# Optimization experiments

Hardware: AMD Instinct MI355X
Metric: run time of the kernel (lower is better)

The kernel has to match this reference:

```python
import jax, jax.numpy as jnp
import numpy as np

D_MODEL = 1024
NUM_HEADS = 16
D_K = D_MODEL // NUM_HEADS
THETA = 10000.0
SEQ = 2048
BATCH = 2


def _rope(t, positions):
    # t: [b, h, s, d_k]; positions: [s]
    half = D_K // 2
    freqs = 1.0 / (THETA ** (jnp.arange(0, D_K, 2, dtype=jnp.float32) / D_K))  # [half]
    angles = positions.astype(jnp.float32)[:, None] * freqs[None, :]  # [s, half]
    cos = jnp.cos(angles)  # [s, half]
    sin = jnp.sin(angles)
    tr = t.reshape(t.shape[:-1] + (half, 2))  # pairs are (even, odd) interleaved
    x1, x2 = tr[..., 0], tr[..., 1]
    r1 = x1 * cos - x2 * sin
    r2 = x1 * sin + x2 * cos
    return jnp.stack([r1, r2], axis=-1).reshape(t.shape)


def setup_inputs() -> dict:
    key = jax.random.key(0)
    ks = jax.random.split(key, 5)
    std = float(np.sqrt(2.0 / (D_MODEL + D_MODEL)))
    return {
        "x": jax.random.normal(ks[0], (BATCH, SEQ, D_MODEL), dtype=jnp.float32),
        "token_positions": jnp.arange(SEQ, dtype=jnp.int64 if jax.config.jax_enable_x64 else jnp.int32),
        "wq": std * jax.random.normal(ks[1], (D_MODEL, D_MODEL), dtype=jnp.float32),
        "wk": std * jax.random.normal(ks[2], (D_MODEL, D_MODEL), dtype=jnp.float32),
        "wv": std * jax.random.normal(ks[3], (D_MODEL, D_MODEL), dtype=jnp.float32),
        "wo": std * jax.random.normal(ks[4], (D_MODEL, D_MODEL), dtype=jnp.float32),
    }


def reference(x, token_positions, wq, wk, wv, wo):
    b, s, _ = x.shape
    # projections: weight is (d_out, d_in), y = x @ W^T
    def proj(w):
        y = jnp.einsum('bsd,od->bso', x, w)
        return y.reshape(b, s, NUM_HEADS, D_K).transpose(0, 2, 1, 3)  # [b,h,s,dk]
    Q, K, V = proj(wq), proj(wk), proj(wv)
    Q = _rope(Q, token_positions)
    K = _rope(K, token_positions)
    scale = 1.0 / jnp.sqrt(jnp.asarray(D_K, dtype=x.dtype))
    scores = jnp.einsum('bhqd,bhkd->bhqk', Q, K) * scale  # [b,h,s,s]
    causal = jnp.tril(jnp.ones((s, s), dtype=bool))
    scores = jnp.where(causal, scores, jnp.asarray(-jnp.inf, dtype=scores.dtype))
    attn = jax.nn.softmax(scores, axis=-1)
    out = jnp.einsum('bhqk,bhkd->bhqd', attn, V)  # [b,h,s,dk]
    out = out.transpose(0, 2, 1, 3).reshape(b, s, D_MODEL)
    return jnp.einsum('bsd,od->bso', out, wo)
```

## Files before the change

### kernel.cpp

```cpp
#include <hip/hip_runtime.h>
#include <hip/hip_bf16.h>
#include <math.h>

#define BATCH  2
#define SEQ    2048
#define DMODEL 1024
#define NHEADS 16
#define DK     64

typedef __hip_bfloat16 bf16;
typedef short s16x8 __attribute__((ext_vector_type(8)));
typedef float f32x4 __attribute__((ext_vector_type(4)));

union P8 { int4 i4; s16x8 v; short s[8]; };

static __device__ __forceinline__ unsigned short f2bu(float f) {
    bf16 h = __float2bfloat16(f);
    return *reinterpret_cast<unsigned short*>(&h);
}

static __device__ __forceinline__ void gll16(const void* g, void* l) {
    __builtin_amdgcn_global_load_lds(
        (const __attribute__((address_space(1))) unsigned int*)g,
        (__attribute__((address_space(3))) unsigned int*)l, 16, 0, 0);
}

#define BAR()    __builtin_amdgcn_s_barrier()
#define LGKM0()  do { asm volatile("s_waitcnt lgkmcnt(0)" ::: "memory"); \
                      __builtin_amdgcn_sched_barrier(0); } while (0)
#define WVM(n)   do { asm volatile("s_waitcnt vmcnt(" #n ")" ::: "memory"); \
                      __builtin_amdgcn_sched_barrier(0); } while (0)

__global__ __launch_bounds__(256) void conv_k(
    const float* __restrict__ x, const float* __restrict__ wq,
    const float* __restrict__ wk, const float* __restrict__ wv,
    const float* __restrict__ wo, bf16* __restrict__ dst)
{
    const size_t e0 = ((size_t)blockIdx.x * 256 + threadIdx.x) << 3;
    const float* src;
    bf16* d;
    if (e0 < (size_t)4194304) { src = x + e0; d = dst + e0; }
    else {
        const size_t r = e0 - 4194304;
        const int wsel = (int)(r >> 20);
        const size_t off = r & 1048575;
        src = (wsel == 0 ? wq : wsel == 1 ? wk : wsel == 2 ? wv : wo) + off;
        d = dst + 4194304 + ((size_t)wsel << 20) + off;
    }
    const float4 a = *(const float4*)src;
    const float4 b = *(const float4*)(src + 4);
    P8 p;
    p.s[0] = (short)f2bu(a.x); p.s[1] = (short)f2bu(a.y);
    p.s[2] = (short)f2bu(a.z); p.s[3] = (short)f2bu(a.w);
    p.s[4] = (short)f2bu(b.x); p.s[5] = (short)f2bu(b.y);
    p.s[6] = (short)f2bu(b.z); p.s[7] = (short)f2bu(b.w);
    *(int4*)d = p.i4;
}

__global__ __launch_bounds__(512, 2) void gemm_qkv(
    const bf16* __restrict__ Ab, const bf16* __restrict__ Wb,
    bf16* __restrict__ O0, bf16* __restrict__ O1, bf16* __restrict__ O2)
{
    __shared__ __align__(16) short As[2][256 * 64];
    __shared__ __align__(16) short Ws[2][256 * 64];
    const int tid  = threadIdx.x;
    const int wid  = tid >> 6;
    const int lane = tid & 63;
    const int ln   = lane & 15;
    const int quad = lane >> 4;
    const int wr   = wid >> 2;
    const int wc   = wid & 3;
    const int swz  = ln & 7;

    const int orig = blockIdx.x;
    const int wg = (orig & 7) * 24 + (orig >> 3);
    const int m_base = (wg & 15) << 8;
    const int nz = wg >> 4;
    const int z  = nz >> 2;
    const int n_base = (nz & 3) << 8;
    const bf16* Wz = Wb + ((size_t)z << 20);

    const int lrw = lane >> 3;
    const int lcs = ((lane & 7) ^ lrw) << 3;

    auto stageHalf = [&](int b, int kt, int q) {
        if (kt >= 16) return;
        const int rs = (q & 1) * 128 + wid * 16;
        if (q < 2) {
            const size_t src = (size_t)(m_base + rs + lrw) * DMODEL
                             + (size_t)(kt * 64 + lcs);
            short* d = &As[b][rs * 64];
            gll16(Ab + src,              d);
            gll16(Ab + src + 8 * DMODEL, d + 8 * 64);
        } else {
            const size_t src = (size_t)(n_base + rs + lrw) * DMODEL
                             + (size_t)(kt * 64 + lcs);
            short* d = &Ws[b][rs * 64];
            gll16(Wz + src,              d);
            gll16(Wz + src + 8 * DMODEL, d + 8 * 64);
        }
    };

    const f32x4 zero4 = {0.f, 0.f, 0.f, 0.f};
    f32x4 acc[8][4];
    #pragma unroll
    for (int i = 0; i < 8; ++i)
        #pragma unroll
        for (int j = 0; j < 4; ++j) acc[i][j] = zero4;

    s16x8 af[4][2], bw01[2][2], bw23[2][2];

    auto readA = [&](const short* Sb, int mg) {
        #pragma unroll
        for (int mi = 0; mi < 4; ++mi)
            #pragma unroll
            for (int kk = 0; kk < 2; ++kk)
                af[mi][kk] = *(const s16x8*)&Sb[
                    (wr * 128 + mg * 64 + 16 * mi + ln) * 64 +
                    ((((kk << 2) + quad) ^ swz) << 3)];
    };
    auto readB = [&](const short* Sb, int np, s16x8 (&bwp)[2][2]) {
        #pragma unroll
        for (int nj = 0; nj < 2; ++nj)
            #pragma unroll
            for (int kk = 0; kk < 2; ++kk)
                bwp[nj][kk] = *(const s16x8*)&Sb[
                    (wc * 64 + np * 32 + 16 * nj + ln) * 64 +
                    ((((kk << 2) + quad) ^ swz) << 3)];
    };
    auto mmac = [&](int mg, int np, const s16x8 (&bwp)[2][2]) {
        #pragma unroll
        for (int mi = 0; mi < 4; ++mi)
            #pragma unroll
            for (int nj = 0; nj < 2; ++nj)
                #pragma unroll
                for (int kk = 0; kk < 2; ++kk)
                    acc[mg * 4 + mi][np * 2 + nj] =
                        __builtin_amdgcn_mfma_f32_16x16x32_bf16(
                            af[mi][kk], bwp[nj][kk],
                            acc[mg * 4 + mi][np * 2 + nj], 0, 0, 0);
    };

    stageHalf(0, 0, 0); stageHalf(0, 0, 1);
    stageHalf(0, 0, 2); stageHalf(0, 0, 3);
    stageHalf(1, 1, 0);
    WVM(2);
    BAR();

    #pragma unroll 1
    for (int i = 0; i < 8; ++i) {
        const int ta = 2 * i, tb = 2 * i + 1;
        readA(As[0], 0); readB(Ws[0], 0, bw01);
        stageHalf(1, tb, 1);
        BAR(); LGKM0();
        __builtin_amdgcn_s_setprio(1); mmac(0, 0, bw01);
        __builtin_amdgcn_s_setprio(0); BAR();
        readB(Ws[0], 1, bw23);
        stageHalf(1, tb, 2);
        BAR(); LGKM0();
        __builtin_amdgcn_s_setprio(1); mmac(0, 1, bw23);
        __builtin_amdgcn_s_setprio(0); BAR();
        readA(As[0], 1);
        stageHalf(1, tb, 3);
        BAR(); LGKM0();
        __builtin_amdgcn_s_setprio(1); mmac(1, 0, bw01);
        __builtin_amdgcn_s_setprio(0); BAR();
        stageHalf(0, ta + 2, 0);
        if (i < 7) { WVM(2); } else { WVM(0); }
        BAR();
        __builtin_amdgcn_s_setprio(1); mmac(1, 1, bw23);
        __builtin_amdgcn_s_setprio(0); BAR();
        readA(As[1], 0); readB(Ws[1], 0, bw01);
        stageHalf(0, ta + 2, 1);
        BAR(); LGKM0();
        __builtin_amdgcn_s_setprio(1); mmac(0, 0, bw01);
        __builtin_amdgcn_s_setprio(0); BAR();
        readB(Ws[1], 1, bw23);
        stageHalf(0, ta + 2, 2);
        BAR(); LGKM0();
        __builtin_amdgcn_s_setprio(1); mmac(0, 1, bw23);
        __builtin_amdgcn_s_setprio(0); BAR();
        readA(As[1], 1);
        stageHalf(0, ta + 2, 3);
        BAR(); LGKM0();
        __builtin_amdgcn_s_setprio(1); mmac(1, 0, bw01);
        __builtin_amdgcn_s_setprio(0); BAR();
        stageHalf(1, tb + 2, 0);
        if (i < 7) { WVM(2); } else { WVM(0); }
        BAR();
        __builtin_amdgcn_s_setprio(1); mmac(1, 1, bw23);
        __builtin_amdgcn_s_setprio(0); BAR();
    }

    if (z < 2) {
        bf16* C = (z == 0) ? O0 : O1;
        const float qs = (z == 0) ? 0.125f * 1.44269504089f : 1.0f;
        const int h = (n_base >> 6) + wc;
        const float sgn = (ln & 1) ? 1.0f : -1.0f;
        float freq[4];
        #pragma unroll
        for (int nj = 0; nj < 4; ++nj)
            freq[nj] = exp2f(-(float)((16 * nj + ln) >> 1) * 0.4152410119f);
        #pragma unroll
        for (int mi = 0; mi < 8; ++mi) {
            #pragma unroll
            for (int r = 0; r < 4; ++r) {
                const int m = m_base + wr * 128 + 16 * mi + quad * 4 + r;
                const int b = m >> 11, s = m & (SEQ - 1);
                const float fs = (float)s;
                float sn[4], cs[4];
                #pragma unroll
                for (int nj = 0; nj < 4; ++nj)
                    __sincosf(fs * freq[nj], &sn[nj], &cs[nj]);
                bf16* row = C + (((size_t)(b * NHEADS + h) * SEQ) + s) * DK;
                #pragma unroll
                for (int nj = 0; nj < 4; ++nj) {
                    const float v = acc[mi][nj][r];
                    const float p = __shfl_xor(v, 1, 64);
                    row[16 * nj + ln] =
                        __float2bfloat16((v * cs[nj] + sgn * p * sn[nj]) * qs);
                }
            }
        }
    } else {
        #pragma unroll
        for (int nj = 0; nj < 4; ++nj) {
            const int n = n_base + wc * 64 + 16 * nj + ln;
            const int h = n >> 6, d = n & (DK - 1);
            #pragma unroll
            for (int mi = 0; mi < 8; ++mi) {
                const int m0v = m_base + wr * 128 + 16 * mi + quad * 4;
                const int b = m0v >> 11, s0 = m0v & (SEQ - 1);
                ushort4 pk;
                pk.x = f2bu(acc[mi][nj][0]); pk.y = f2bu(acc[mi][nj][1]);
                pk.z = f2bu(acc[mi][nj][2]); pk.w = f2bu(acc[mi][nj][3]);
                *(ushort4*)(O2 + (((size_t)(b * NHEADS + h) * DK) + d) * SEQ + s0) = pk;
            }
        }
    }
}

__global__ __launch_bounds__(256) void gemm_wo(
    const bf16* __restrict__ Ab, const bf16* __restrict__ Wb,
    float* __restrict__ Of)
{
    __shared__ __align__(16) short As[64 * 64];
    __shared__ __align__(16) short Ws2[128 * 64];
    const int tid  = threadIdx.x;
    const int w    = tid >> 6;
    const int lane = tid & 63;
    const int ln   = lane & 15;
    const int quad = lane >> 4;
    const int id   = blockIdx.x;
    const int m_base = (id & 63) << 6;
    const int n_base = (id >> 6) << 7;

    const int lrw = lane >> 3;
    const int lcs = ((lane & 7) ^ lrw) << 3;
    const int am = m_base + 16 * w + lrw;
    short* ldsA = &As[1024 * w];
    const size_t wbase = (size_t)(n_base + 32 * w + lrw) * DMODEL + lcs;
    short* ldsW = &Ws2[2048 * w];

    const f32x4 zero4 = {0.f, 0.f, 0.f, 0.f};
    f32x4 acc[2][4];
    #pragma unroll
    for (int i = 0; i < 2; ++i)
        #pragma unroll
        for (int j = 0; j < 4; ++j) acc[i][j] = zero4;

    const int mo = (w >> 1) << 5, no = (w & 1) << 6;
    const int swz = ln & 7;

    for (int k0 = 0; k0 < DMODEL; k0 += 64) {
        const int hh = k0 >> 6;
        __syncthreads();
        #pragma unroll
        for (int t = 0; t < 2; ++t) {
            const int m = am + t * 8;
            const int b = m >> 11, s = m & (SEQ - 1);
            gll16(Ab + (((size_t)(b * NHEADS + hh) * SEQ) + s) * DK + lcs,
                  ldsA + t * 512);
        }
        #pragma unroll
        for (int t = 0; t < 4; ++t)
            gll16(Wb + wbase + (size_t)t * 8 * DMODEL + k0, ldsW + t * 512);
        __syncthreads();
        #pragma unroll
        for (int t = 0; t < 2; ++t) {
            const int co = (((t << 2) + quad) ^ swz) << 3;
            s16x8 af[2], bw[4];
            #pragma unroll
            for (int i = 0; i < 2; ++i)
                af[i] = *(const s16x8*)&As[(mo + 16 * i + ln) * 64 + co];
            #pragma unroll
            for (int j = 0; j < 4; ++j)
                bw[j] = *(const s16x8*)&Ws2[(no + 16 * j + ln) * 64 + co];
            #pragma unroll
            for (int mi = 0; mi < 2; ++mi)
                #pragma unroll
                for (int ni = 0; ni < 4; ++ni)
                    acc[mi][ni] = __builtin_amdgcn_mfma_f32_16x16x32_bf16(
                        af[mi], bw[ni], acc[mi][ni], 0, 0, 0);
        }
    }

    #pragma unroll
    for (int mi = 0; mi < 2; ++mi)
        #pragma unroll
        for (int ni = 0; ni < 4; ++ni) {
            const int n = n_base + no + 16 * ni + ln;
            #pragma unroll
            for (int r = 0; r < 4; ++r) {
                const int m = m_base + mo + 16 * mi + quad * 4 + r;
                Of[(size_t)m * DMODEL + n] = acc[mi][ni][r];
            }
        }
}

__global__ __launch_bounds__(256) void attn_k(bf16* __restrict__ Q,
                                              const bf16* __restrict__ Kg,
                                              const bf16* __restrict__ VT)
{
    __shared__ __align__(16) short Ks[2][64 * 64];
    __shared__ __align__(16) short Vs[2][64 * 64];
    __shared__ __align__(16) short PT[4 * 16 * 64];
    const int tid  = threadIdx.x;
    const int w    = tid >> 6;
    const int lane = tid & 63;
    const int ln   = lane & 15;
    const int quad = lane >> 4;
    const int bh = blockIdx.x & 31;
    const int qt = 31 - (blockIdx.x >> 5);
    const size_t base = (size_t)bh * (SEQ * DK);
    const int srow = tid >> 2;
    const int sc   = (tid & 3) << 4;
    const int qrow = qt * 64 + 16 * w + ln;

    const int sr7 = srow & 7;
    const int wofs0 = srow * 64 + ((((sc >> 3)    ) ^ sr7) << 3);
    const int wofs1 = srow * 64 + ((((sc >> 3) | 1) ^ sr7) << 3);
    const int l7 = ln & 7;
    const int rof0 = ln * 64 + ((quad ^ l7) << 3);
    const int rof1 = ln * 64 + (((4 | quad) ^ l7) << 3);
    short* PTw = &PT[w << 10];

    P8 qa0, qa1;
    {
        const bf16* qsrc = Q + base + (size_t)qrow * DK + quad * 8;
        qa0.i4 = *(const int4*)(qsrc);
        qa1.i4 = *(const int4*)(qsrc + 32);
    }
    const f32x4 zero4 = {0.f, 0.f, 0.f, 0.f};
    f32x4 o[4];
    #pragma unroll
    for (int mt = 0; mt < 4; ++mt) o[mt] = zero4;
    float lsum = 0.f;

    P8 kk[2], vv[2];
    auto loadTile = [&](int t) {
        const bf16* ksrc = Kg + base + (size_t)(t * 64 + srow) * DK + sc;
        kk[0].i4 = *(const int4*)(ksrc);
        kk[1].i4 = *(const int4*)(ksrc + 8);
        const bf16* vsrc = VT + base + (size_t)srow * SEQ + t * 64 + sc;
        vv[0].i4 = *(const int4*)(vsrc);
        vv[1].i4 = *(const int4*)(vsrc + 8);
    };

    loadTile(0);
    {
        short* Kb = Ks[0];
        short* Vb = Vs[0];
        *(s16x8*)&Kb[wofs0] = kk[0].v;
        *(s16x8*)&Kb[wofs1] = kk[1].v;
        *(s16x8*)&Vb[wofs0] = vv[0].v;
        *(s16x8*)&Vb[wofs1] = vv[1].v;
    }
    if (qt > 0) loadTile(1);
    LGKM0();
    BAR();

    #pragma unroll 1
    for (int t = 0; t <= qt; ++t) {
        const int p = t & 1;
        if (t < qt) {
            short* Kb = Ks[p ^ 1];
            short* Vb = Vs[p ^ 1];
            *(s16x8*)&Kb[wofs0] = kk[0].v;
            *(s16x8*)&Kb[wofs1] = kk[1].v;
            *(s16x8*)&Vb[wofs0] = vv[0].v;
            *(s16x8*)&Vb[wofs1] = vv[1].v;
            if (t + 2 <= qt) loadTile(t + 2);
        }

        const short* Kp = Ks[p];
        const short* Vp = Vs[p];
        f32x4 sf[4];
        __builtin_amdgcn_s_setprio(1);
        #pragma unroll
        for (int mt = 0; mt < 4; ++mt) {
            sf[mt] = zero4;
            s16x8 ka  = *(const s16x8*)&Kp[mt * 1024 + rof0];
            s16x8 kb2 = *(const s16x8*)&Kp[mt * 1024 + rof1];
            sf[mt] = __builtin_amdgcn_mfma_f32_16x16x32_bf16(ka,  qa0.v, sf[mt], 0, 0, 0);
            sf[mt] = __builtin_amdgcn_mfma_f32_16x16x32_bf16(kb2, qa1.v, sf[mt], 0, 0, 0);
        }
        __builtin_amdgcn_s_setprio(0);

        if (t == qt) {
            #pragma unroll
            for (int mt = 0; mt < 4; ++mt)
                #pragma unroll
                for (int r = 0; r < 4; ++r)
                    if (t * 64 + 16 * mt + quad * 4 + r > qrow) sf[mt][r] = -INFINITY;
        }
        #pragma unroll
        for (int mt = 0; mt < 4; ++mt)
            #pragma unroll
            for (int r = 0; r < 4; ++r) {
                sf[mt][r] = exp2f(sf[mt][r]);
                lsum += sf[mt][r];
            }

        #pragma unroll
        for (int mt = 0; mt < 4; ++mt) {
            ushort4 pk;
            pk.x = f2bu(sf[mt][0]); pk.y = f2bu(sf[mt][1]);
            pk.z = f2bu(sf[mt][2]); pk.w = f2bu(sf[mt][3]);
            *(ushort4*)&PTw[ln * 64 + ((((2 * mt) | (quad >> 1)) ^ l7) << 3)
                            + ((quad & 1) << 2)] = pk;
        }

        s16x8 pa0 = *(const s16x8*)&PTw[rof0];
        s16x8 pa1 = *(const s16x8*)&PTw[rof1];
        __builtin_amdgcn_s_setprio(1);
        #pragma unroll
        for (int mt = 0; mt < 4; ++mt) {
            s16x8 va0 = *(const s16x8*)&Vp[mt * 1024 + rof0];
            s16x8 va1 = *(const s16x8*)&Vp[mt * 1024 + rof1];
            o[mt] = __builtin_amdgcn_mfma_f32_16x16x32_bf16(va0, pa0, o[mt], 0, 0, 0);
            o[mt] = __builtin_amdgcn_mfma_f32_16x16x32_bf16(va1, pa1, o[mt], 0, 0, 0);
        }
        __builtin_amdgcn_s_setprio(0);

        if (t < qt) { LGKM0(); BAR(); }
    }

    lsum += __shfl_xor(lsum, 16, 64);
    lsum += __shfl_xor(lsum, 32, 64);
    const float inv = 1.0f / lsum;
    #pragma unroll
    for (int mt = 0; mt < 4; ++mt) {
        ushort4 st;
        st.x = f2bu(o[mt][0] * inv); st.y = f2bu(o[mt][1] * inv);
        st.z = f2bu(o[mt][2] * inv); st.w = f2bu(o[mt][3] * inv);
        *(ushort4*)(Q + base + (size_t)qrow * DK + 16 * mt + quad * 4) = st;
    }
}

extern "C" void kernel_launch(void* const* d_in, const int* in_sizes, int n_in,
                              void* d_out, int out_size, void* d_ws, size_t ws_size,
                              hipStream_t stream)
{
    const float* x  = (const float*)d_in[0];
    const float* wq = (const float*)d_in[2];
    const float* wk = (const float*)d_in[3];
    const float* wv = (const float*)d_in[4];
    const float* wo = (const float*)d_in[5];

    bf16* wsb   = (bf16*)d_ws;
    bf16* xb    = wsb;
    bf16* wqkvb = wsb + ((size_t)4 << 20);
    bf16* wob   = wsb + ((size_t)7 << 20);
    bf16* Qw    = wsb + ((size_t)8 << 20);
    bf16* Kw    = wsb + ((size_t)12 << 20);
    bf16* VTw   = wsb + ((size_t)16 << 20);

    conv_k<<<4096, 256, 0, stream>>>(x, wq, wk, wv, wo, wsb);
    gemm_qkv<<<192, 512, 0, stream>>>(xb, wqkvb, Qw, Kw, VTw);
    attn_k<<<1024, 256, 0, stream>>>(Qw, Kw, VTw);
    gemm_wo<<<512, 256, 0, stream>>>(Qw, wob, (float*)d_out);
}
```

Before: 182.9 us.

## Load K/V fragments directly from global memory in attention, drop LDS staging

The attention kernel no longer stages K and V tiles through double-buffered shared memory with block barriers. Each wave now loads its own MFMA operand fragments for K and V straight from global memory (relying on L2/cache for reuse across the four waves), and the launch bounds ask for four blocks per CU. This removes LDS writes, LDS reads and per-iteration barriers, but each wave now fetches the full K/V tile itself, and the loads are issued inside the loop without software prefetch, so global latency may be exposed.

```diff
diff --git a/kernel.cpp b/kernel.cpp
--- a/kernel.cpp
+++ b/kernel.cpp
@@ -318,12 +318,10 @@
         }
 }
 
-__global__ __launch_bounds__(256) void attn_k(bf16* __restrict__ Q,
-                                              const bf16* __restrict__ Kg,
-                                              const bf16* __restrict__ VT)
+__global__ __launch_bounds__(256, 4) void attn_k(bf16* __restrict__ Q,
+                                                 const bf16* __restrict__ Kg,
+                                                 const bf16* __restrict__ VT)
 {
-    __shared__ __align__(16) short Ks[2][64 * 64];
-    __shared__ __align__(16) short Vs[2][64 * 64];
     __shared__ __align__(16) short PT[4 * 16 * 64];
     const int tid  = threadIdx.x;
     const int w    = tid >> 6;
@@ -333,13 +331,8 @@
     const int bh = blockIdx.x & 31;
     const int qt = 31 - (blockIdx.x >> 5);
     const size_t base = (size_t)bh * (SEQ * DK);
-    const int srow = tid >> 2;
-    const int sc   = (tid & 3) << 4;
     const int qrow = qt * 64 + 16 * w + ln;
 
-    const int sr7 = srow & 7;
-    const int wofs0 = srow * 64 + ((((sc >> 3)    ) ^ sr7) << 3);
-    const int wofs1 = srow * 64 + ((((sc >> 3) | 1) ^ sr7) << 3);
     const int l7 = ln & 7;
     const int rof0 = ln * 64 + ((quad ^ l7) << 3);
     const int rof1 = ln * 64 + (((4 | quad) ^ l7) << 3);
@@ -357,55 +350,36 @@
     for (int mt = 0; mt < 4; ++mt) o[mt] = zero4;
     float lsum = 0.f;
 
-    P8 kk[2], vv[2];
-    auto loadTile = [&](int t) {
-        const bf16* ksrc = Kg + base + (size_t)(t * 64 + srow) * DK + sc;
-        kk[0].i4 = *(const int4*)(ksrc);
-        kk[1].i4 = *(const int4*)(ksrc + 8);
-        const bf16* vsrc = VT + base + (size_t)srow * SEQ + t * 64 + sc;
-        vv[0].i4 = *(const int4*)(vsrc);
-        vv[1].i4 = *(const int4*)(vsrc + 8);
-    };
-
-    loadTile(0);
-    {
-        short* Kb = Ks[0];
-        short* Vb = Vs[0];
-        *(s16x8*)&Kb[wofs0] = kk[0].v;
-        *(s16x8*)&Kb[wofs1] = kk[1].v;
-        *(s16x8*)&Vb[wofs0] = vv[0].v;
-        *(s16x8*)&Vb[wofs1] = vv[1].v;
-    }
-    if (qt > 0) loadTile(1);
-    LGKM0();
-    BAR();
+    const bf16* kp0 = Kg + base + (size_t)ln * DK + quad * 8;
+    const bf16* vp0 = VT + base + (size_t)ln * SEQ + quad * 8;
 
     #pragma unroll 1
     for (int t = 0; t <= qt; ++t) {
-        const int p = t & 1;
-        if (t < qt) {
-            short* Kb = Ks[p ^ 1];
-            short* Vb = Vs[p ^ 1];
-            *(s16x8*)&Kb[wofs0] = kk[0].v;
-            *(s16x8*)&Kb[wofs1] = kk[1].v;
-            *(s16x8*)&Vb[wofs0] = vv[0].v;
-            *(s16x8*)&Vb[wofs1] = vv[1].v;
-            if (t + 2 <= qt) loadTile(t + 2);
-        }
-
-        const short* Kp = Ks[p];
-        const short* Vp = Vs[p];
+        const bf16* kp = kp0 + (size_t)t * 64 * DK;
+        P8 kf[4][2];
+        #pragma unroll
+        for (int mt = 0; mt < 4; ++mt) {
+            kf[mt][0].i4 = *(const int4*)(kp + (size_t)mt * 16 * DK);
+            kf[mt][1].i4 = *(const int4*)(kp + (size_t)mt * 16 * DK + 32);
+        }
+
         f32x4 sf[4];
         __builtin_amdgcn_s_setprio(1);
         #pragma unroll
         for (int mt = 0; mt < 4; ++mt) {
             sf[mt] = zero4;
-            s16x8 ka  = *(const s16x8*)&Kp[mt * 1024 + rof0];
-            s16x8 kb2 = *(const s16x8*)&Kp[mt * 1024 + rof1];
-            sf[mt] = __builtin_amdgcn_mfma_f32_16x16x32_bf16(ka,  qa0.v, sf[mt], 0, 0, 0);
-            sf[mt] = __builtin_amdgcn_mfma_f32_16x16x32_bf16(kb2, qa1.v, sf[mt], 0, 0, 0);
+            sf[mt] = __builtin_amdgcn_mfma_f32_16x16x32_bf16(kf[mt][0].v, qa0.v, sf[mt], 0, 0, 0);
+            sf[mt] = __builtin_amdgcn_mfma_f32_16x16x32_bf16(kf[mt][1].v, qa1.v, sf[mt], 0, 0, 0);
         }
         __builtin_amdgcn_s_setprio(0);
+
+        const bf16* vp = vp0 + t * 64;
+        P8 vf[4][2];
+        #pragma unroll
+        for (int mt = 0; mt < 4; ++mt) {
+            vf[mt][0].i4 = *(const int4*)(vp + (size_t)mt * 16 * SEQ);
+            vf[mt][1].i4 = *(const int4*)(vp + (size_t)mt * 16 * SEQ + 32);
+        }
 
         if (t == qt) {
             #pragma unroll
@@ -436,14 +410,10 @@
         __builtin_amdgcn_s_setprio(1);
         #pragma unroll
         for (int mt = 0; mt < 4; ++mt) {
-            s16x8 va0 = *(const s16x8*)&Vp[mt * 1024 + rof0];
-            s16x8 va1 = *(const s16x8*)&Vp[mt * 1024 + rof1];
-            o[mt] = __builtin_amdgcn_mfma_f32_16x16x32_bf16(va0, pa0, o[mt], 0, 0, 0);
-            o[mt] = __builtin_amdgcn_mfma_f32_16x16x32_bf16(va1, pa1, o[mt], 0, 0, 0);
+            o[mt] = __builtin_amdgcn_mfma_f32_16x16x32_bf16(vf[mt][0].v, pa0, o[mt], 0, 0, 0);
+            o[mt] = __builtin_amdgcn_mfma_f32_16x16x32_bf16(vf[mt][1].v, pa1, o[mt], 0, 0, 0);
         }
         __builtin_amdgcn_s_setprio(0);
-
-        if (t < qt) { LGKM0(); BAR(); }
     }
 
     lsum += __shfl_xor(lsum, 16, 64);
```

Result: slower. 283.3 us (+54.9%).

## Double-buffer LDS staging with direct global-to-LDS loads in wo GEMM and attention

Applied to the files above, without the earlier changes.

The output-projection GEMM now double-buffers its A and W tiles in LDS and prefetches two k-steps ahead with global_load_lds, using vmcnt waits instead of a full sync around each load. The attention kernel swaps its register-staged K/V copies for direct global-to-LDS loads into the same double buffer, drops the setprio hints, and reorders query tiles so long and short causal tiles are interleaved across the grid. This is meant to overlap memory latency with MFMA work and balance causal load, at the cost of more LDS per block and extra barriers.

```diff
diff --git a/kernel.cpp b/kernel.cpp
--- a/kernel.cpp
+++ b/kernel.cpp
@@ -244,8 +244,8 @@
     const bf16* __restrict__ Ab, const bf16* __restrict__ Wb,
     float* __restrict__ Of)
 {
-    __shared__ __align__(16) short As[64 * 64];
-    __shared__ __align__(16) short Ws2[128 * 64];
+    __shared__ __align__(16) short As[2][64 * 64];
+    __shared__ __align__(16) short Ws2[2][128 * 64];
     const int tid  = threadIdx.x;
     const int w    = tid >> 6;
     const int lane = tid & 63;
@@ -258,9 +258,24 @@
     const int lrw = lane >> 3;
     const int lcs = ((lane & 7) ^ lrw) << 3;
     const int am = m_base + 16 * w + lrw;
-    short* ldsA = &As[1024 * w];
     const size_t wbase = (size_t)(n_base + 32 * w + lrw) * DMODEL + lcs;
-    short* ldsW = &Ws2[2048 * w];
+
+    auto stageK = [&](int b, int kt) {
+        const int hh = kt;
+        short* ldsA = &As[b][1024 * w];
+        short* ldsW = &Ws2[b][2048 * w];
+        #pragma unroll
+        for (int t = 0; t < 2; ++t) {
+            const int m = am + t * 8;
+            const int bb = m >> 11, s = m & (SEQ - 1);
+            gll16(Ab + (((size_t)(bb * NHEADS + hh) * SEQ) + s) * DK + lcs,
+                  ldsA + t * 512);
+        }
+        #pragma unroll
+        for (int t = 0; t < 4; ++t)
+            gll16(Wb + wbase + (size_t)t * 8 * DMODEL + (kt << 6),
+                  ldsW + t * 512);
+    };
 
     const f32x4 zero4 = {0.f, 0.f, 0.f, 0.f};
     f32x4 acc[2][4];
@@ -272,30 +287,26 @@
     const int mo = (w >> 1) << 5, no = (w & 1) << 6;
     const int swz = ln & 7;
 
-    for (int k0 = 0; k0 < DMODEL; k0 += 64) {
-        const int hh = k0 >> 6;
-        __syncthreads();
-        #pragma unroll
-        for (int t = 0; t < 2; ++t) {
-            const int m = am + t * 8;
-            const int b = m >> 11, s = m & (SEQ - 1);
-            gll16(Ab + (((size_t)(b * NHEADS + hh) * SEQ) + s) * DK + lcs,
-                  ldsA + t * 512);
-        }
-        #pragma unroll
-        for (int t = 0; t < 4; ++t)
-            gll16(Wb + wbase + (size_t)t * 8 * DMODEL + k0, ldsW + t * 512);
-        __syncthreads();
+    stageK(0, 0);
+    stageK(1, 1);
+
+    #pragma unroll 1
+    for (int kt = 0; kt < 16; ++kt) {
+        const int p = kt & 1;
+        if (kt + 1 < 16) { WVM(6); } else { WVM(0); }
+        BAR();
+        const short* Ap = As[p];
+        const short* Wp = Ws2[p];
         #pragma unroll
         for (int t = 0; t < 2; ++t) {
             const int co = (((t << 2) + quad) ^ swz) << 3;
             s16x8 af[2], bw[4];
             #pragma unroll
             for (int i = 0; i < 2; ++i)
-                af[i] = *(const s16x8*)&As[(mo + 16 * i + ln) * 64 + co];
+                af[i] = *(const s16x8*)&Ap[(mo + 16 * i + ln) * 64 + co];
             #pragma unroll
             for (int j = 0; j < 4; ++j)
-                bw[j] = *(const s16x8*)&Ws2[(no + 16 * j + ln) * 64 + co];
+                bw[j] = *(const s16x8*)&Wp[(no + 16 * j + ln) * 64 + co];
             #pragma unroll
             for (int mi = 0; mi < 2; ++mi)
                 #pragma unroll
@@ -303,6 +314,8 @@
                     acc[mi][ni] = __builtin_amdgcn_mfma_f32_16x16x32_bf16(
                         af[mi], bw[ni], acc[mi][ni], 0, 0, 0);
         }
+        BAR();
+        if (kt + 2 < 16) stageK(p, kt + 2);
     }
 
     #pragma unroll
@@ -331,15 +344,26 @@
     const int ln   = lane & 15;
     const int quad = lane >> 4;
     const int bh = blockIdx.x & 31;
-    const int qt = 31 - (blockIdx.x >> 5);
+    const int row = blockIdx.x >> 5;
+    const int bk = row & 7, bg = row >> 3;
+    const int qt = (bg == 0) ? 31 - bk : (bg == 1) ? 15 - bk
+                 : (bg == 2) ? 16 + bk : bk;
     const size_t base = (size_t)bh * (SEQ * DK);
-    const int srow = tid >> 2;
-    const int sc   = (tid & 3) << 4;
     const int qrow = qt * 64 + 16 * w + ln;
 
-    const int sr7 = srow & 7;
-    const int wofs0 = srow * 64 + ((((sc >> 3)    ) ^ sr7) << 3);
-    const int wofs1 = srow * 64 + ((((sc >> 3) | 1) ^ sr7) << 3);
+    const int lrw = lane >> 3;
+    const int lcs = ((lane & 7) ^ lrw) << 3;
+    auto stageT = [&](int b, int t) {
+        #pragma unroll
+        for (int i = 0; i < 2; ++i) {
+            const int r0 = w * 16 + i * 8;
+            gll16(Kg + base + (size_t)(t * 64 + r0 + lrw) * DK + lcs,
+                  &Ks[b][r0 * 64]);
+            gll16(VT + base + (size_t)(r0 + lrw) * SEQ + t * 64 + lcs,
+                  &Vs[b][r0 * 64]);
+        }
+    };
+
     const int l7 = ln & 7;
     const int rof0 = ln * 64 + ((quad ^ l7) << 3);
     const int rof1 = ln * 64 + (((4 | quad) ^ l7) << 3);
@@ -357,46 +381,19 @@
     for (int mt = 0; mt < 4; ++mt) o[mt] = zero4;
     float lsum = 0.f;
 
-    P8 kk[2], vv[2];
-    auto loadTile = [&](int t) {
-        const bf16* ksrc = Kg + base + (size_t)(t * 64 + srow) * DK + sc;
-        kk[0].i4 = *(const int4*)(ksrc);
-        kk[1].i4 = *(const int4*)(ksrc + 8);
-        const bf16* vsrc = VT + base + (size_t)srow * SEQ + t * 64 + sc;
-        vv[0].i4 = *(const int4*)(vsrc);
-        vv[1].i4 = *(const int4*)(vsrc + 8);
-    };
-
-    loadTile(0);
-    {
-        short* Kb = Ks[0];
-        short* Vb = Vs[0];
-        *(s16x8*)&Kb[wofs0] = kk[0].v;
-        *(s16x8*)&Kb[wofs1] = kk[1].v;
-        *(s16x8*)&Vb[wofs0] = vv[0].v;
-        *(s16x8*)&Vb[wofs1] = vv[1].v;
-    }
-    if (qt > 0) loadTile(1);
-    LGKM0();
-    BAR();
+    const int nt = qt + 1;
+    stageT(0, 0);
+    stageT(1, nt > 1 ? 1 : 0);
 
     #pragma unroll 1
-    for (int t = 0; t <= qt; ++t) {
+    for (int t = 0; t < nt; ++t) {
         const int p = t & 1;
-        if (t < qt) {
-            short* Kb = Ks[p ^ 1];
-            short* Vb = Vs[p ^ 1];
-            *(s16x8*)&Kb[wofs0] = kk[0].v;
-            *(s16x8*)&Kb[wofs1] = kk[1].v;
-            *(s16x8*)&Vb[wofs0] = vv[0].v;
-            *(s16x8*)&Vb[wofs1] = vv[1].v;
-            if (t + 2 <= qt) loadTile(t + 2);
-        }
-
+        if (t + 1 < nt) { WVM(4); } else { WVM(0); }
+        BAR();
         const short* Kp = Ks[p];
         const short* Vp = Vs[p];
+
         f32x4 sf[4];
-        __builtin_amdgcn_s_setprio(1);
         #pragma unroll
         for (int mt = 0; mt < 4; ++mt) {
             sf[mt] = zero4;
@@ -405,7 +402,6 @@
             sf[mt] = __builtin_amdgcn_mfma_f32_16x16x32_bf16(ka,  qa0.v, sf[mt], 0, 0, 0);
             sf[mt] = __builtin_amdgcn_mfma_f32_16x16x32_bf16(kb2, qa1.v, sf[mt], 0, 0, 0);
         }
-        __builtin_amdgcn_s_setprio(0);
 
         if (t == qt) {
             #pragma unroll
@@ -433,7 +429,6 @@
 
         s16x8 pa0 = *(const s16x8*)&PTw[rof0];
         s16x8 pa1 = *(const s16x8*)&PTw[rof1];
-        __builtin_amdgcn_s_setprio(1);
         #pragma unroll
         for (int mt = 0; mt < 4; ++mt) {
             s16x8 va0 = *(const s16x8*)&Vp[mt * 1024 + rof0];
@@ -441,9 +436,9 @@
             o[mt] = __builtin_amdgcn_mfma_f32_16x16x32_bf16(va0, pa0, o[mt], 0, 0, 0);
             o[mt] = __builtin_amdgcn_mfma_f32_16x16x32_bf16(va1, pa1, o[mt], 0, 0, 0);
         }
-        __builtin_amdgcn_s_setprio(0);
-
-        if (t < qt) { LGKM0(); BAR(); }
+
+        BAR();
+        if (t + 2 < nt) stageT(p, t + 2);
     }
 
     lsum += __shfl_xor(lsum, 16, 64);
```

After: 174.7 us. 1.05x faster.
